# Kernel tuning notes

Hardware: AMD Instinct MI355X
Metric: run time of the kernel (lower is better)

## Reference

```python
import jax, jax.numpy as jnp
import numpy as np

D_MODEL = 1024
N_HEADS = 16
HEAD_DIM = D_MODEL // N_HEADS
SPARSITY = 0.5  # torch.rand(...) < sparsity_factor -> True means masked (disallowed)


def setup_inputs() -> dict:
    key = jax.random.key(0)
    ks = jax.random.split(key, 12)
    B, S, D = 2, 2048, D_MODEL
    query = jax.random.normal(ks[0], (B, S, D), dtype=jnp.float32)
    key_t = jax.random.normal(ks[1], (B, S, D), dtype=jnp.float32)
    value = jax.random.normal(ks[2], (B, S, D), dtype=jnp.float32)
    # per-forward random boolean mask, materialized deterministically here
    mask = jax.random.uniform(ks[3], (B, S, S)) < SPARSITY
    scale = 1.0 / np.sqrt(D)
    Wq = jax.random.uniform(ks[4], (D, D), jnp.float32, -scale, scale)
    Wk = jax.random.uniform(ks[5], (D, D), jnp.float32, -scale, scale)
    Wv = jax.random.uniform(ks[6], (D, D), jnp.float32, -scale, scale)
    Wo = jax.random.uniform(ks[7], (D, D), jnp.float32, -scale, scale)
    bq = jnp.zeros((D,), jnp.float32)
    bk = jnp.zeros((D,), jnp.float32)
    bv = jnp.zeros((D,), jnp.float32)
    bo = jnp.zeros((D,), jnp.float32)
    return {"query": query, "key": key_t, "value": value, "mask": mask,
            "Wq": Wq, "Wk": Wk, "Wv": Wv, "Wo": Wo,
            "bq": bq, "bk": bk, "bv": bv, "bo": bo}


def reference(query, key, value, mask, Wq, Wk, Wv, Wo, bq, bk, bv, bo):
    B, S, D = query.shape
    H, hd = N_HEADS, HEAD_DIM
    # in-projections (torch uses x @ W.T + b)
    q = (query @ Wq.T + bq).reshape(B, S, H, hd).transpose(0, 2, 1, 3)  # (B,H,S,hd)
    k = (key @ Wk.T + bk).reshape(B, S, H, hd).transpose(0, 2, 1, 3)
    v = (value @ Wv.T + bv).reshape(B, S, H, hd).transpose(0, 2, 1, 3)
    scores = jnp.einsum('bhqd,bhkd->bhqk', q, k) / jnp.sqrt(jnp.float32(hd))
    # bool mask: True = disallowed; broadcast over heads
    scores = jnp.where(mask[:, None, :, :], -jnp.inf, scores)
    attn = jax.nn.softmax(scores, axis=-1)  # dropout inactive at eval
    out = jnp.einsum('bhqk,bhkd->bhqd', attn, v)  # (B,H,S,hd)
    out = out.transpose(0, 2, 1, 3).reshape(B, S, D)
    return out @ Wo.T + bo
```

## Files before the change

kernel.cpp:

```cpp
#include <hip/hip_runtime.h>
#include <stdint.h>

#define MTOK   4096
#define DMODEL 1024
#define SEQ    2048
#define NH     16
#define HD     64
#define LDK    72
#define QSCL   0.18033688f
#define NWORDS (2 * SEQ * SEQ / 64)

typedef _Float16 h8  __attribute__((ext_vector_type(8)));
typedef _Float16 h4  __attribute__((ext_vector_type(4)));
typedef _Float16 h2  __attribute__((ext_vector_type(2)));
typedef __fp16   fp16x2 __attribute__((ext_vector_type(2)));
typedef float    f16v __attribute__((ext_vector_type(16)));
typedef float    f4  __attribute__((ext_vector_type(4)));

typedef __attribute__((address_space(1))) const unsigned int g_u32;
typedef __attribute__((address_space(3))) unsigned int       l_u32;

__device__ __forceinline__ void g2l16(const void* g, void* l) {
    __builtin_amdgcn_global_load_lds((g_u32*)(unsigned long long)g,
                                     (l_u32*)(unsigned int)(unsigned long long)l,
                                     16, 0, 0);
}

__device__ __forceinline__ unsigned pkrtz_u(float a, float b) {
    fp16x2 r = __builtin_amdgcn_cvt_pkrtz(a, b);
    return __builtin_bit_cast(unsigned, r);
}

#if __has_builtin(__builtin_amdgcn_exp2f)
#define E2(x) __builtin_amdgcn_exp2f(x)
#else
#define E2(x) exp2f(x)
#endif

__global__ __launch_bounds__(256) void prep_kernel(
    const float* __restrict__ s0, const float* __restrict__ s1,
    const float* __restrict__ s2, const float* __restrict__ s3,
    const float* __restrict__ s4, const float* __restrict__ s5,
    const float* __restrict__ s6,
    _Float16* __restrict__ d0, _Float16* __restrict__ d1,
    _Float16* __restrict__ d2, _Float16* __restrict__ d3,
    _Float16* __restrict__ d4, _Float16* __restrict__ d5,
    _Float16* __restrict__ d6,
    const unsigned char* __restrict__ mb, const unsigned int* __restrict__ mu,
    unsigned long long* __restrict__ mout) {
    const int z = blockIdx.y;
    const int gid = blockIdx.x * 256 + threadIdx.x;
    const int stride = gridDim.x * 256;
    if (z < 7) {
        const float* s = (z == 0) ? s0 : (z == 1) ? s1 : (z == 2) ? s2
                       : (z == 3) ? s3 : (z == 4) ? s4 : (z == 5) ? s5 : s6;
        _Float16* d = (z == 0) ? d0 : (z == 1) ? d1 : (z == 2) ? d2
                    : (z == 3) ? d3 : (z == 4) ? d4 : (z == 5) ? d5 : d6;
        const int n4 = (z < 3) ? (MTOK * DMODEL / 4) : (DMODEL * DMODEL / 4);
        for (int i = gid; i < n4; i += stride) {
            float4 v = ((const float4*)s)[i];
            h4 o = {(_Float16)v.x, (_Float16)v.y, (_Float16)v.z, (_Float16)v.w};
            ((h4*)d)[i] = o;
        }
    } else {
        __shared__ int wsum[4];
        int cnt = 0;
        const uchar4* mp4 = (const uchar4*)mb;
#pragma unroll
        for (int i = 0; i < 8; ++i) {
            uchar4 v = mp4[threadIdx.x * 8 + i];
            cnt += (v.x != 0) + (v.y != 0) + (v.z != 0) + (v.w != 0);
        }
#pragma unroll
        for (int off = 32; off > 0; off >>= 1) cnt += __shfl_down(cnt, off, 64);
        if ((threadIdx.x & 63) == 0) wsum[threadIdx.x >> 6] = cnt;
        __syncthreads();
        const int byteflag = (wsum[0] + wsum[1] + wsum[2] + wsum[3]) > 2500;

        for (int w = gid; w < NWORDS; w += stride) {
            unsigned long long bits = 0ull;
            if (byteflag) {
                const uint4* p = (const uint4*)(mb + (size_t)w * 64);
#pragma unroll
                for (int i = 0; i < 4; ++i) {
                    uint4 v = p[i];
                    unsigned dw[4] = {v.x, v.y, v.z, v.w};
#pragma unroll
                    for (int j = 0; j < 4; ++j) {
                        unsigned d = dw[j];
                        unsigned nib = (unsigned)((d & 0xFFu) != 0)
                                     | ((unsigned)((d & 0xFF00u) != 0) << 1)
                                     | ((unsigned)((d & 0xFF0000u) != 0) << 2)
                                     | ((unsigned)((d >> 24) != 0) << 3);
                        bits |= (unsigned long long)nib << (i * 16 + j * 4);
                    }
                }
            } else {
                const uint4* p = (const uint4*)(mu + (size_t)w * 64);
#pragma unroll
                for (int i = 0; i < 16; ++i) {
                    uint4 v = p[i];
                    unsigned nib = (unsigned)(v.x != 0u)
                                 | ((unsigned)(v.y != 0u) << 1)
                                 | ((unsigned)(v.z != 0u) << 2)
                                 | ((unsigned)(v.w != 0u) << 3);
                    bits |= (unsigned long long)nib << (i * 4);
                }
            }
            mout[w] = bits;
        }
    }
}

template <int MODE, int BN>
__device__ __forceinline__ void gemm16_body(const _Float16* __restrict__ A,
                                            const _Float16* __restrict__ W,
                                            const float* __restrict__ bias,
                                            void* __restrict__ outv,
                                            float scale) {
    __shared__ __align__(16) _Float16 Asb[128 * 32];
    __shared__ __align__(16) _Float16 Bsb[BN * 32];
    constexpr int NJ = BN / 32;
    const int tid = threadIdx.x;
    const int wv = tid >> 6, lane = tid & 63;
    const int l15 = lane & 15, g = lane >> 4;
    const int wy = wv >> 1, wx = wv & 1;
    const int m0 = blockIdx.x * 128, n0 = blockIdx.y * BN;

    f4 acc[4][NJ];
#pragma unroll
    for (int i = 0; i < 4; ++i)
#pragma unroll
        for (int j = 0; j < NJ; ++j) acc[i][j] = (f4){0.f, 0.f, 0.f, 0.f};

    const int oA0 = tid * 16, oA1 = (256 + tid) * 16;
    const int rA0 = oA0 >> 6, cA0 = oA0 & 63;
    const int rA1 = oA1 >> 6, cA1 = oA1 & 63;
    const char* Ab = (const char*)A;
    const char* Wb = (const char*)W;

    for (int kt = 0; kt < 32; ++kt) {
        const int k0b = kt * 64;
        __syncthreads();
        g2l16(Ab + (size_t)(m0 + rA0) * 2048 + k0b + cA0, (char*)Asb + oA0);
        g2l16(Ab + (size_t)(m0 + rA1) * 2048 + k0b + cA1, (char*)Asb + oA1);
        g2l16(Wb + (size_t)(n0 + rA0) * 2048 + k0b + cA0, (char*)Bsb + oA0);
        if (BN == 128)
            g2l16(Wb + (size_t)(n0 + rA1) * 2048 + k0b + cA1, (char*)Bsb + oA1);
        __syncthreads();

        h8 af[4], bf[NJ];
#pragma unroll
        for (int t = 0; t < 4; ++t)
            af[t] = *(const h8*)(Asb + (wy * 64 + t * 16 + l15) * 32 + g * 8);
#pragma unroll
        for (int t = 0; t < NJ; ++t)
            bf[t] = *(const h8*)(Bsb + (wx * (BN / 2) + t * 16 + l15) * 32 + g * 8);
#pragma unroll
        for (int i = 0; i < 4; ++i)
#pragma unroll
            for (int j = 0; j < NJ; ++j) {
                if (MODE == 2)
                    acc[i][j] = __builtin_amdgcn_mfma_f32_16x16x32_f16(
                        bf[j], af[i], acc[i][j], 0, 0, 0);
                else
                    acc[i][j] = __builtin_amdgcn_mfma_f32_16x16x32_f16(
                        af[i], bf[j], acc[i][j], 0, 0, 0);
            }
    }

#pragma unroll
    for (int j = 0; j < NJ; ++j) {
#pragma unroll
        for (int i = 0; i < 4; ++i) {
            if (MODE == 2) {
                const int m = m0 + wy * 64 + i * 16 + l15;
                const int b = m >> 11, s = m & 2047;
#pragma unroll
                for (int r = 0; r < 4; ++r) {
                    const int n = n0 + wx * (BN / 2) + j * 16 + g * 4 + r;
                    const int h = n >> 6, d = n & 63;
                    ((_Float16*)outv)[(((size_t)(b * NH + h)) * HD + d) * SEQ + s] =
                        (_Float16)(acc[i][j][r] + bias[n]);
                }
            } else {
                const int n = n0 + wx * (BN / 2) + j * 16 + l15;
                const float bb = bias[n];
                const int mbase = m0 + wy * 64 + i * 16 + g * 4;
                if (MODE == 1) {
                    const int h = n >> 6, d = n & 63;
#pragma unroll
                    for (int r = 0; r < 4; ++r) {
                        const int m = mbase + r;
                        const int b = m >> 11, s = m & 2047;
                        ((_Float16*)outv)[(((size_t)(b * NH + h)) * SEQ + s) * HD + d] =
                            (_Float16)((acc[i][j][r] + bb) * scale);
                    }
                } else {
#pragma unroll
                    for (int r = 0; r < 4; ++r)
                        ((float*)outv)[(size_t)(mbase + r) * DMODEL + n] =
                            acc[i][j][r] + bb;
                }
            }
        }
    }
}

__global__ __launch_bounds__(256) void qkv_gemm16_kernel(
    const _Float16* __restrict__ xq, const _Float16* __restrict__ xk,
    const _Float16* __restrict__ xv,
    const _Float16* __restrict__ Wq, const _Float16* __restrict__ Wk,
    const _Float16* __restrict__ Wv,
    const float* __restrict__ bq, const float* __restrict__ bk,
    const float* __restrict__ bv,
    _Float16* __restrict__ q_out, _Float16* __restrict__ k_out,
    _Float16* __restrict__ vt_out) {
    const int z = blockIdx.z;
    if (z == 0)      gemm16_body<1, 128>(xq, Wq, bq, (void*)q_out, QSCL);
    else if (z == 1) gemm16_body<1, 128>(xk, Wk, bk, (void*)k_out, 1.0f);
    else             gemm16_body<2, 128>(xv, Wv, bv, (void*)vt_out, 1.0f);
}

__global__ __launch_bounds__(256) void out_gemm16_kernel(
    const _Float16* __restrict__ X, const _Float16* __restrict__ W,
    const float* __restrict__ bias, float* __restrict__ out) {
    gemm16_body<0, 64>(X, W, bias, (void*)out, 1.0f);
}

__global__ __launch_bounds__(256, 4) void attn_kernel(
    const _Float16* __restrict__ Q, const _Float16* __restrict__ K,
    const _Float16* __restrict__ Vt,
    const unsigned long long* __restrict__ mbits,
    _Float16* __restrict__ out) {
    __shared__ __align__(16) _Float16 Ks[2][64 * LDK];
    __shared__ __align__(16) _Float16 Vs[2][64 * LDK];

    const int tid = threadIdx.x;
    const int wv = tid >> 6, lane = tid & 63;
    const int l31 = lane & 31, hi = lane >> 5;
    const int q0 = blockIdx.x * 128;
    const int bh = blockIdx.y;
    const int b = bh >> 4, h = bh & 15;
    const size_t bho = (size_t)bh * (SEQ * HD);
    const int qrow = q0 + wv * 32 + l31;

    h8 qf[4];
    const _Float16* qp = Q + bho + (size_t)qrow * HD;
#pragma unroll
    for (int ks = 0; ks < 4; ++ks) qf[ks] = *(const h8*)(qp + ks * 16 + hi * 8);

    f16v Ot[2];
#pragma unroll
    for (int mt = 0; mt < 2; ++mt)
#pragma unroll
        for (int r = 0; r < 16; ++r) Ot[mt][r] = 0.f;
    float l_r = 0.f;

    const int sr = tid >> 2;
    const int scol = (tid & 3) * 16;
    const _Float16* kg = K + bho;
    const _Float16* vg = Vt + bho;
    const unsigned long long* mrow =
        mbits + ((size_t)b * SEQ + qrow) * (SEQ / 64);

    h8 kr0 = *(const h8*)(kg + (size_t)sr * HD + scol);
    h8 kr1 = *(const h8*)(kg + (size_t)sr * HD + scol + 8);
    h8 vr0 = *(const h8*)(vg + (size_t)sr * SEQ + scol);
    h8 vr1 = *(const h8*)(vg + (size_t)sr * SEQ + scol + 8);
    uint2 mw = *(const uint2*)(mrow);
    *(h8*)(&Ks[0][sr * LDK + scol])     = kr0;
    *(h8*)(&Ks[0][sr * LDK + scol + 8]) = kr1;
    *(h8*)(&Vs[0][sr * LDK + scol])     = vr0;
    *(h8*)(&Vs[0][sr * LDK + scol + 8]) = vr1;
    __syncthreads();

    for (int kt = 0; kt < 32; ++kt) {
        const int cur = kt & 1;
        uint2 mw_n;
        if (kt < 31) {
            const int k0n = (kt + 1) * 64;
            kr0 = *(const h8*)(kg + (size_t)(k0n + sr) * HD + scol);
            kr1 = *(const h8*)(kg + (size_t)(k0n + sr) * HD + scol + 8);
            vr0 = *(const h8*)(vg + (size_t)sr * SEQ + k0n + scol);
            vr1 = *(const h8*)(vg + (size_t)sr * SEQ + k0n + scol + 8);
            mw_n = *(const uint2*)(mrow + kt + 1);
        }

        f16v sc0, sc1;
#pragma unroll
        for (int r = 0; r < 16; ++r) { sc0[r] = 0.f; sc1[r] = 0.f; }
#pragma unroll
        for (int ks = 0; ks < 4; ++ks) {
            h8 kf0 = *(const h8*)(&Ks[cur][l31 * LDK + ks * 16 + hi * 8]);
            h8 kf1 = *(const h8*)(&Ks[cur][(32 + l31) * LDK + ks * 16 + hi * 8]);
            sc0 = __builtin_amdgcn_mfma_f32_32x32x16_f16(kf0, qf[ks], sc0, 0, 0, 0);
            sc1 = __builtin_amdgcn_mfma_f32_32x32x16_f16(kf1, qf[ks], sc1, 0, 0, 0);
        }

        float ps = 0.f;
        unsigned Du[2][4][2];
#pragma unroll
        for (int mt = 0; mt < 2; ++mt) {
            const unsigned w = mt ? mw.y : mw.x;
            const f16v& s = mt ? sc1 : sc0;
#pragma unroll
            for (int g4 = 0; g4 < 4; ++g4) {
                const int sh = g4 * 8 + hi * 4;
                float p0 = E2(((w >> (sh + 0)) & 1u) ? -1e30f : s[g4 * 4 + 0]);
                float p1 = E2(((w >> (sh + 1)) & 1u) ? -1e30f : s[g4 * 4 + 1]);
                float p2 = E2(((w >> (sh + 2)) & 1u) ? -1e30f : s[g4 * 4 + 2]);
                float p3 = E2(((w >> (sh + 3)) & 1u) ? -1e30f : s[g4 * 4 + 3]);
                Du[mt][g4][0] = pkrtz_u(p0, p1);
                Du[mt][g4][1] = pkrtz_u(p2, p3);
                ps += p0 + p1 + p2 + p3;
            }
        }
        l_r += ps;

        h8 pf[4];
#pragma unroll
        for (int ks = 0; ks < 4; ++ks) {
            const int mtc = ks >> 1, base = (ks & 1) * 2;
            const unsigned A0 = Du[mtc][base][0],     A1 = Du[mtc][base][1];
            const unsigned B0 = Du[mtc][base + 1][0], B1 = Du[mtc][base + 1][1];
            const unsigned s0 = hi ? A0 : B0;
            const unsigned s1 = hi ? A1 : B1;
            const unsigned o0 = hi ? B0 : A0;
            const unsigned o1 = hi ? B1 : A1;
            const unsigned r0 = (unsigned)__shfl_xor((int)s0, 32, 64);
            const unsigned r1 = (unsigned)__shfl_xor((int)s1, 32, 64);
            uint4 fv;
            fv.x = hi ? r0 : o0;
            fv.y = hi ? r1 : o1;
            fv.z = hi ? o0 : r0;
            fv.w = hi ? o1 : r1;
            pf[ks] = __builtin_bit_cast(h8, fv);
        }

#pragma unroll
        for (int ks = 0; ks < 4; ++ks) {
            h8 vf0 = *(const h8*)(&Vs[cur][l31 * LDK + ks * 16 + hi * 8]);
            h8 vf1 = *(const h8*)(&Vs[cur][(32 + l31) * LDK + ks * 16 + hi * 8]);
            Ot[0] = __builtin_amdgcn_mfma_f32_32x32x16_f16(vf0, pf[ks], Ot[0], 0, 0, 0);
            Ot[1] = __builtin_amdgcn_mfma_f32_32x32x16_f16(vf1, pf[ks], Ot[1], 0, 0, 0);
        }

        if (kt < 31) {
            const int nxt = cur ^ 1;
            *(h8*)(&Ks[nxt][sr * LDK + scol])     = kr0;
            *(h8*)(&Ks[nxt][sr * LDK + scol + 8]) = kr1;
            *(h8*)(&Vs[nxt][sr * LDK + scol])     = vr0;
            *(h8*)(&Vs[nxt][sr * LDK + scol + 8]) = vr1;
            mw = mw_n;
        }
        __syncthreads();
    }

    l_r += __shfl_xor(l_r, 32);
    const float inv = 1.0f / l_r;
    _Float16* op = out + ((size_t)b * SEQ + qrow) * DMODEL + h * HD;
#pragma unroll
    for (int mt = 0; mt < 2; ++mt)
#pragma unroll
        for (int g4 = 0; g4 < 4; ++g4) {
            const int d = mt * 32 + g4 * 8 + hi * 4;
            h4 ov = {(_Float16)(Ot[mt][g4 * 4 + 0] * inv),
                     (_Float16)(Ot[mt][g4 * 4 + 1] * inv),
                     (_Float16)(Ot[mt][g4 * 4 + 2] * inv),
                     (_Float16)(Ot[mt][g4 * 4 + 3] * inv)};
            *(h4*)(op + d) = ov;
        }
}

extern "C" void kernel_launch(void* const* d_in, const int* in_sizes, int n_in,
                              void* d_out, int out_size, void* d_ws, size_t ws_size,
                              hipStream_t stream) {
    const float* query = (const float*)d_in[0];
    const float* key_  = (const float*)d_in[1];
    const float* value = (const float*)d_in[2];
    const void*  mask  = d_in[3];
    const float* Wq = (const float*)d_in[4];
    const float* Wk = (const float*)d_in[5];
    const float* Wv = (const float*)d_in[6];
    const float* Wo = (const float*)d_in[7];
    const float* bq = (const float*)d_in[8];
    const float* bk = (const float*)d_in[9];
    const float* bv = (const float*)d_in[10];
    const float* bo = (const float*)d_in[11];

    char* ws = (char*)d_ws;
    _Float16* xq  = (_Float16*)(ws + 256);
    _Float16* xk  = xq + (size_t)MTOK * DMODEL;
    _Float16* xv  = xk + (size_t)MTOK * DMODEL;
    _Float16* Wqh = xv + (size_t)MTOK * DMODEL;
    _Float16* Wkh = Wqh + (size_t)DMODEL * DMODEL;
    _Float16* Wvh = Wkh + (size_t)DMODEL * DMODEL;
    _Float16* Woh = Wvh + (size_t)DMODEL * DMODEL;
    _Float16* q_ws  = Woh + (size_t)DMODEL * DMODEL;
    _Float16* k_ws  = q_ws + (size_t)MTOK * DMODEL;
    _Float16* vt_ws = k_ws + (size_t)MTOK * DMODEL;
    _Float16* a_ws  = vt_ws + (size_t)MTOK * DMODEL;
    unsigned long long* mb_ws =
        (unsigned long long*)(a_ws + (size_t)MTOK * DMODEL);

    prep_kernel<<<dim3(1024, 8), 256, 0, stream>>>(
        query, key_, value, Wq, Wk, Wv, Wo, xq, xk, xv, Wqh, Wkh, Wvh, Woh,
        (const unsigned char*)mask, (const unsigned int*)mask, mb_ws);

    dim3 gqkv(MTOK / 128, DMODEL / 128, 3);
    qkv_gemm16_kernel<<<gqkv, 256, 0, stream>>>(xq, xk, xv, Wqh, Wkh, Wvh,
                                                bq, bk, bv, q_ws, k_ws, vt_ws);

    dim3 gattn(SEQ / 128, 2 * NH);
    attn_kernel<<<gattn, 256, 0, stream>>>(q_ws, k_ws, vt_ws, mb_ws, a_ws);

    dim3 gout(MTOK / 128, DMODEL / 64);
    out_gemm16_kernel<<<gout, 256, 0, stream>>>(a_ws, Woh, bo, (float*)d_out);
}
```

Before: 282.7 us.

## Split key range across two wave groups per attention block and merge via LDS

The attention block grows to 512 threads, with two groups of four waves each covering half of the key sequence for the same 128 queries. Each group keeps its own double-buffered K/V tiles. At the end, the second group writes its partial output and row sums to LDS, and the first group adds them before normalizing. This doubles resident waves and halves the serial key loop to improve latency hiding. The cost is an extra LDS reduction pass and higher shared memory use per block.

```diff
diff --git a/kernel.cpp b/kernel.cpp
--- a/kernel.cpp
+++ b/kernel.cpp
@@ -9,10 +9,10 @@
 #define LDK    72
 #define QSCL   0.18033688f
 #define NWORDS (2 * SEQ * SEQ / 64)
+#define GRP_B  36864
 
 typedef _Float16 h8  __attribute__((ext_vector_type(8)));
 typedef _Float16 h4  __attribute__((ext_vector_type(4)));
-typedef _Float16 h2  __attribute__((ext_vector_type(2)));
 typedef __fp16   fp16x2 __attribute__((ext_vector_type(2)));
 typedef float    f16v __attribute__((ext_vector_type(16)));
 typedef float    f4  __attribute__((ext_vector_type(4)));
@@ -228,22 +228,28 @@
     gemm16_body<0, 64>(X, W, bias, (void*)out, 1.0f);
 }
 
-__global__ __launch_bounds__(256, 4) void attn_kernel(
+__global__ __launch_bounds__(512, 4) void attn_kernel(
     const _Float16* __restrict__ Q, const _Float16* __restrict__ K,
     const _Float16* __restrict__ Vt,
     const unsigned long long* __restrict__ mbits,
     _Float16* __restrict__ out) {
-    __shared__ __align__(16) _Float16 Ks[2][64 * LDK];
-    __shared__ __align__(16) _Float16 Vs[2][64 * LDK];
+    __shared__ __align__(16) char smem[2 * GRP_B];
 
     const int tid = threadIdx.x;
     const int wv = tid >> 6, lane = tid & 63;
+    const int g2 = wv >> 2, wq = wv & 3;
     const int l31 = lane & 31, hi = lane >> 5;
     const int q0 = blockIdx.x * 128;
     const int bh = blockIdx.y;
     const int b = bh >> 4, h = bh & 15;
     const size_t bho = (size_t)bh * (SEQ * HD);
-    const int qrow = q0 + wv * 32 + l31;
+    const int qrow = q0 + wq * 32 + l31;
+    const int qloc = wq * 32 + l31;
+
+    _Float16* Ksg = (_Float16*)(smem + g2 * GRP_B);
+    _Float16* Vsg = Ksg + 2 * 64 * LDK;
+    float* Om = (float*)(smem + GRP_B);
+    float* lm = Om + 64 * 132;
 
     h8 qf[4];
     const _Float16* qp = Q + bho + (size_t)qrow * HD;
@@ -257,34 +263,38 @@
         for (int r = 0; r < 16; ++r) Ot[mt][r] = 0.f;
     float l_r = 0.f;
 
-    const int sr = tid >> 2;
-    const int scol = (tid & 3) * 16;
+    const int gt = tid & 255;
+    const int sr = gt >> 2;
+    const int scol = (gt & 3) * 16;
     const _Float16* kg = K + bho;
     const _Float16* vg = Vt + bho;
     const unsigned long long* mrow =
-        mbits + ((size_t)b * SEQ + qrow) * (SEQ / 64);
-
-    h8 kr0 = *(const h8*)(kg + (size_t)sr * HD + scol);
-    h8 kr1 = *(const h8*)(kg + (size_t)sr * HD + scol + 8);
-    h8 vr0 = *(const h8*)(vg + (size_t)sr * SEQ + scol);
-    h8 vr1 = *(const h8*)(vg + (size_t)sr * SEQ + scol + 8);
+        mbits + ((size_t)b * SEQ + qrow) * (SEQ / 64) + g2 * 16;
+    const int kbase = g2 * 16 * 64;
+
+    h8 kr0 = *(const h8*)(kg + (size_t)(kbase + sr) * HD + scol);
+    h8 kr1 = *(const h8*)(kg + (size_t)(kbase + sr) * HD + scol + 8);
+    h8 vr0 = *(const h8*)(vg + (size_t)sr * SEQ + kbase + scol);
+    h8 vr1 = *(const h8*)(vg + (size_t)sr * SEQ + kbase + scol + 8);
     uint2 mw = *(const uint2*)(mrow);
-    *(h8*)(&Ks[0][sr * LDK + scol])     = kr0;
-    *(h8*)(&Ks[0][sr * LDK + scol + 8]) = kr1;
-    *(h8*)(&Vs[0][sr * LDK + scol])     = vr0;
-    *(h8*)(&Vs[0][sr * LDK + scol + 8]) = vr1;
+    *(h8*)(&Ksg[sr * LDK + scol])     = kr0;
+    *(h8*)(&Ksg[sr * LDK + scol + 8]) = kr1;
+    *(h8*)(&Vsg[sr * LDK + scol])     = vr0;
+    *(h8*)(&Vsg[sr * LDK + scol + 8]) = vr1;
     __syncthreads();
 
-    for (int kt = 0; kt < 32; ++kt) {
-        const int cur = kt & 1;
+    for (int it = 0; it < 16; ++it) {
+        const int cur = it & 1;
+        _Float16* Ksc = Ksg + cur * 64 * LDK;
+        _Float16* Vsc = Vsg + cur * 64 * LDK;
         uint2 mw_n;
-        if (kt < 31) {
-            const int k0n = (kt + 1) * 64;
+        if (it < 15) {
+            const int k0n = kbase + (it + 1) * 64;
             kr0 = *(const h8*)(kg + (size_t)(k0n + sr) * HD + scol);
             kr1 = *(const h8*)(kg + (size_t)(k0n + sr) * HD + scol + 8);
             vr0 = *(const h8*)(vg + (size_t)sr * SEQ + k0n + scol);
             vr1 = *(const h8*)(vg + (size_t)sr * SEQ + k0n + scol + 8);
-            mw_n = *(const uint2*)(mrow + kt + 1);
+            mw_n = *(const uint2*)(mrow + it + 1);
         }
 
         f16v sc0, sc1;
@@ -292,8 +302,8 @@
         for (int r = 0; r < 16; ++r) { sc0[r] = 0.f; sc1[r] = 0.f; }
 #pragma unroll
         for (int ks = 0; ks < 4; ++ks) {
-            h8 kf0 = *(const h8*)(&Ks[cur][l31 * LDK + ks * 16 + hi * 8]);
-            h8 kf1 = *(const h8*)(&Ks[cur][(32 + l31) * LDK + ks * 16 + hi * 8]);
+            h8 kf0 = *(const h8*)(&Ksc[l31 * LDK + ks * 16 + hi * 8]);
+            h8 kf1 = *(const h8*)(&Ksc[(32 + l31) * LDK + ks * 16 + hi * 8]);
             sc0 = __builtin_amdgcn_mfma_f32_32x32x16_f16(kf0, qf[ks], sc0, 0, 0, 0);
             sc1 = __builtin_amdgcn_mfma_f32_32x32x16_f16(kf1, qf[ks], sc1, 0, 0, 0);
         }
@@ -340,37 +350,53 @@
 
 #pragma unroll
         for (int ks = 0; ks < 4; ++ks) {
-            h8 vf0 = *(const h8*)(&Vs[cur][l31 * LDK + ks * 16 + hi * 8]);
-            h8 vf1 = *(const h8*)(&Vs[cur][(32 + l31) * LDK + ks * 16 + hi * 8]);
+            h8 vf0 = *(const h8*)(&Vsc[l31 * LDK + ks * 16 + hi * 8]);
+            h8 vf1 = *(const h8*)(&Vsc[(32 + l31) * LDK + ks * 16 + hi * 8]);
             Ot[0] = __builtin_amdgcn_mfma_f32_32x32x16_f16(vf0, pf[ks], Ot[0], 0, 0, 0);
             Ot[1] = __builtin_amdgcn_mfma_f32_32x32x16_f16(vf1, pf[ks], Ot[1], 0, 0, 0);
         }
 
-        if (kt < 31) {
-            const int nxt = cur ^ 1;
-            *(h8*)(&Ks[nxt][sr * LDK + scol])     = kr0;
-            *(h8*)(&Ks[nxt][sr * LDK + scol + 8]) = kr1;
-            *(h8*)(&Vs[nxt][sr * LDK + scol])     = vr0;
-            *(h8*)(&Vs[nxt][sr * LDK + scol + 8]) = vr1;
+        if (it < 15) {
+            const int nxt = (cur ^ 1) * 64 * LDK;
+            *(h8*)(&Ksg[nxt + sr * LDK + scol])     = kr0;
+            *(h8*)(&Ksg[nxt + sr * LDK + scol + 8]) = kr1;
+            *(h8*)(&Vsg[nxt + sr * LDK + scol])     = vr0;
+            *(h8*)(&Vsg[nxt + sr * LDK + scol + 8]) = vr1;
             mw = mw_n;
         }
         __syncthreads();
     }
 
     l_r += __shfl_xor(l_r, 32);
-    const float inv = 1.0f / l_r;
-    _Float16* op = out + ((size_t)b * SEQ + qrow) * DMODEL + h * HD;
-#pragma unroll
-    for (int mt = 0; mt < 2; ++mt)
-#pragma unroll
-        for (int g4 = 0; g4 < 4; ++g4) {
-            const int d = mt * 32 + g4 * 8 + hi * 4;
-            h4 ov = {(_Float16)(Ot[mt][g4 * 4 + 0] * inv),
-                     (_Float16)(Ot[mt][g4 * 4 + 1] * inv),
-                     (_Float16)(Ot[mt][g4 * 4 + 2] * inv),
-                     (_Float16)(Ot[mt][g4 * 4 + 3] * inv)};
-            *(h4*)(op + d) = ov;
-        }
+    if (g2 == 1) {
+#pragma unroll
+        for (int mt = 0; mt < 2; ++mt)
+#pragma unroll
+            for (int g4 = 0; g4 < 4; ++g4) {
+                const int d = mt * 32 + g4 * 8 + hi * 4;
+#pragma unroll
+                for (int r = 0; r < 4; ++r)
+                    Om[(d + r) * 132 + qloc] = Ot[mt][g4 * 4 + r];
+            }
+        if (hi == 0) lm[qloc] = l_r;
+    }
+    __syncthreads();
+    if (g2 == 0) {
+        const float inv = 1.0f / (l_r + lm[qloc]);
+        _Float16* op = out + ((size_t)b * SEQ + qrow) * DMODEL + h * HD;
+#pragma unroll
+        for (int mt = 0; mt < 2; ++mt)
+#pragma unroll
+            for (int g4 = 0; g4 < 4; ++g4) {
+                const int d = mt * 32 + g4 * 8 + hi * 4;
+                float o0 = (Ot[mt][g4 * 4 + 0] + Om[(d + 0) * 132 + qloc]) * inv;
+                float o1 = (Ot[mt][g4 * 4 + 1] + Om[(d + 1) * 132 + qloc]) * inv;
+                float o2 = (Ot[mt][g4 * 4 + 2] + Om[(d + 2) * 132 + qloc]) * inv;
+                float o3 = (Ot[mt][g4 * 4 + 3] + Om[(d + 3) * 132 + qloc]) * inv;
+                h4 ov = {(_Float16)o0, (_Float16)o1, (_Float16)o2, (_Float16)o3};
+                *(h4*)(op + d) = ov;
+            }
+    }
 }
 
 extern "C" void kernel_launch(void* const* d_in, const int* in_sizes, int n_in,
@@ -413,7 +439,7 @@
                                                 bq, bk, bv, q_ws, k_ws, vt_ws);
 
     dim3 gattn(SEQ / 128, 2 * NH);
-    attn_kernel<<<gattn, 256, 0, stream>>>(q_ws, k_ws, vt_ws, mb_ws, a_ws);
+    attn_kernel<<<gattn, 512, 0, stream>>>(q_ws, k_ws, vt_ws, mb_ws, a_ws);
 
     dim3 gout(MTOK / 128, DMODEL / 64);
     out_gemm16_kernel<<<gout, 256, 0, stream>>>(a_ws, Woh, bo, (float*)d_out);
```

Result: no change. 285.1 us (+0.8%).
